# Kernel optimization log

Measured on AMD Instinct MI355X. Metric: run time of the kernel, lower is better.

Reference implementation:

```python
import jax, jax.numpy as jnp
import numpy as np

D_MODEL, D_K, D_V = 1024, 64, 64
B, S = 4, 4096


def setup_inputs() -> dict:
    key = jax.random.key(0)
    ks = jax.random.split(key, 13)
    s = 1.0 / np.sqrt(D_MODEL)
    inp = {
        "q": jax.random.normal(ks[0], (B, S, D_MODEL), jnp.float32),
        "k": jax.random.normal(ks[1], (B, S, D_MODEL), jnp.float32),
        "v": jax.random.normal(ks[2], (B, S, D_MODEL), jnp.float32),
        "mask": jax.random.randint(ks[3], (1, S, S), 0, 2, jnp.int32),
        "Wq": jax.random.normal(ks[4], (D_K, D_MODEL), jnp.float32) * s,
        "bq": jax.random.normal(ks[5], (D_K,), jnp.float32) * s,
        "Wk": jax.random.normal(ks[6], (D_K, D_MODEL), jnp.float32) * s,
        "bk": jax.random.normal(ks[7], (D_K,), jnp.float32) * s,
        "Wv": jax.random.normal(ks[8], (D_V, D_MODEL), jnp.float32) * s,
        "bv": jax.random.normal(ks[9], (D_V,), jnp.float32) * s,
        "Wo": jax.random.normal(ks[10], (D_MODEL, D_V), jnp.float32) / np.sqrt(D_V),
        "bo": jax.random.normal(ks[11], (D_MODEL,), jnp.float32) / np.sqrt(D_V),
    }
    return inp


def reference(q, k, v, mask, Wq, bq, Wk, bk, Wv, bv, Wo, bo):
    # linear projections (torch Linear: x @ W.T + b)
    qh = jnp.einsum("bsd,kd->bsk", q, Wq) + bq   # [B,S,d_k]
    kh = jnp.einsum("bsd,kd->bsk", k, Wk) + bk   # [B,S,d_k]
    vh = jnp.einsum("bsd,vd->bsv", v, Wv) + bv   # [B,S,d_v]
    scale = 1.0 / jnp.sqrt(jnp.float32(D_K))
    scores = jnp.einsum("bqk,bmk->bqm", qh, kh) * scale  # [B,S,S]
    scores = jnp.where(mask == 0, jnp.float32(-1e9), scores)
    attn = jax.nn.softmax(scores, axis=-1)
    out = jnp.einsum("bqm,bmv->bqv", attn, vh)   # [B,S,d_v]
    return jnp.einsum("bqv,dv->bqd", out, Wo) + bo
```

## Files before the change

### kernel.cpp

```cpp
#include <hip/hip_runtime.h>
#include <cmath>

typedef __attribute__((ext_vector_type(8))) short bf16x8;
typedef __attribute__((ext_vector_type(4))) short bf16x4;
typedef __attribute__((ext_vector_type(4))) float f32x4;

constexpr int B_ = 4;
constexpr int S_ = 4096;
constexpr int DM_ = 1024;
constexpr int DK_ = 64;
constexpr int NROW = B_ * S_;

__device__ __forceinline__ short f2bf(float x) {
  union { float f; unsigned u; } c; c.f = x;
  unsigned r = (c.u + 0x7FFF + ((c.u >> 16) & 1)) >> 16;
  return (short)r;
}
__device__ __forceinline__ float bf2f(short h) {
  union { float f; unsigned u; } c; c.u = ((unsigned)(unsigned short)h) << 16;
  return c.f;
}

__global__ __launch_bounds__(256) void prep(
    const int* __restrict__ mask, unsigned long long* __restrict__ bits,
    const float* __restrict__ Wq, const float* __restrict__ Wk,
    const float* __restrict__ Wv, short* __restrict__ wbf) {
  if (blockIdx.x < 1024) {
    const int wid = (blockIdx.x * 256 + threadIdx.x) >> 6;
    const int lane = threadIdx.x & 63;
    const size_t base = (size_t)wid * 4096;
    for (int it = 0; it < 64; ++it) {
      int m = mask[base + it * 64 + lane];
      unsigned long long b = __ballot(m != 0);
      if (lane == 0) bits[(size_t)wid * 64 + it] = b;
    }
  } else {
    const int mat = blockIdx.x - 1024;
    const float* W = mat == 0 ? Wq : (mat == 1 ? Wk : Wv);
    short* dst = wbf + (size_t)mat * DK_ * DM_;
    const int t = threadIdx.x;
#pragma unroll 4
    for (int i = 0; i < 32; ++i) {
      int idx = i * 2048 + t * 8;
      f32x4 a0 = *(const f32x4*)(W + idx);
      f32x4 a1 = *(const f32x4*)(W + idx + 4);
      bf16x8 h;
#pragma unroll
      for (int j = 0; j < 4; ++j) { h[j] = f2bf(a0[j]); h[j + 4] = f2bf(a1[j]); }
      *(bf16x8*)(dst + idx) = h;
    }
  }
}

__global__ __launch_bounds__(256, 3) void proj_mfma(
    const float* __restrict__ q, const float* __restrict__ k,
    const float* __restrict__ v, const short* __restrict__ wbf,
    const float* __restrict__ bq, const float* __restrict__ bk,
    const float* __restrict__ bv,
    short* __restrict__ qh, short* __restrict__ kh, short* __restrict__ vhT) {
  const int mat = blockIdx.z;
  const float* X    = mat == 0 ? q : (mat == 1 ? k : v);
  const short* W    = wbf + (size_t)mat * DK_ * DM_;
  const float* bias = mat == 0 ? bq : (mat == 1 ? bk : bv);

  const int t = threadIdx.x;
  const int row0 = blockIdx.x * 64;
  const int lane = t & 63, w = t >> 6, quad = lane >> 4, l16 = lane & 15;

  const int myrow = row0 + 16 * w + l16;
  const float* xp = X + (size_t)myrow * DM_ + quad * 8;
  const short* wp0 = W + (size_t)l16 * DM_ + quad * 8;
  const short* wp1 = wp0 + 16 * DM_;
  const short* wp2 = wp0 + 32 * DM_;
  const short* wp3 = wp0 + 48 * DM_;

  f32x4 acc[4] = {};
  f32x4 xr[4][4];

#pragma unroll
  for (int pb = 0; pb < 3; ++pb) {
    const float* s = xp + pb * 64;
    xr[pb][0] = *(const f32x4*)(s + 0);
    xr[pb][1] = *(const f32x4*)(s + 4);
    xr[pb][2] = *(const f32x4*)(s + 32);
    xr[pb][3] = *(const f32x4*)(s + 36);
  }

#pragma unroll 4
  for (int ks = 0; ks < 16; ++ks) {
    if (ks < 13) {
      const float* s = xp + (ks + 3) * 64;
      xr[(ks + 3) & 3][0] = *(const f32x4*)(s + 0);
      xr[(ks + 3) & 3][1] = *(const f32x4*)(s + 4);
      xr[(ks + 3) & 3][2] = *(const f32x4*)(s + 32);
      xr[(ks + 3) & 3][3] = *(const f32x4*)(s + 36);
    }

    bf16x8 wf[2][4];
#pragma unroll
    for (int c = 0; c < 2; ++c) {
      wf[c][0] = *(const bf16x8*)(wp0 + ks * 64 + c * 32);
      wf[c][1] = *(const bf16x8*)(wp1 + ks * 64 + c * 32);
      wf[c][2] = *(const bf16x8*)(wp2 + ks * 64 + c * 32);
      wf[c][3] = *(const bf16x8*)(wp3 + ks * 64 + c * 32);
    }

#pragma unroll
    for (int c = 0; c < 2; ++c) {
      f32x4 x0 = xr[ks & 3][2 * c + 0];
      f32x4 x1 = xr[ks & 3][2 * c + 1];
      bf16x8 ahi, alo;
#pragma unroll
      for (int j = 0; j < 4; ++j) {
        short h0 = f2bf(x0[j]); ahi[j] = h0;     alo[j]     = f2bf(x0[j] - bf2f(h0));
        short h1 = f2bf(x1[j]); ahi[j + 4] = h1; alo[j + 4] = f2bf(x1[j] - bf2f(h1));
      }
#pragma unroll
      for (int ct = 0; ct < 4; ++ct) {
        acc[ct] = __builtin_amdgcn_mfma_f32_16x16x32_bf16(ahi, wf[c][ct], acc[ct], 0, 0, 0);
        acc[ct] = __builtin_amdgcn_mfma_f32_16x16x32_bf16(alo, wf[c][ct], acc[ct], 0, 0, 0);
      }
    }
  }

  float bs[4];
#pragma unroll
  for (int ct = 0; ct < 4; ++ct) bs[ct] = bias[16 * ct + l16];

  short* dstq = (mat == 0) ? qh : kh;
#pragma unroll
  for (int ct = 0; ct < 4; ++ct)
#pragma unroll
    for (int reg = 0; reg < 4; ++reg) {
      int r = row0 + 16 * w + quad * 4 + reg;
      int c = 16 * ct + l16;
      short hv = f2bf(acc[ct][reg] + bs[ct]);
      if (mat == 2)
        vhT[((size_t)(r >> 12) * DK_ + c) * S_ + (r & 4095)] = hv;
      else
        dstq[(size_t)r * DK_ + c] = hv;
    }
}

__global__ __launch_bounds__(256) void attn_mfma(
    const short* __restrict__ qh, const short* __restrict__ kh,
    const short* __restrict__ vhT, const unsigned int* __restrict__ mbits,
    float* __restrict__ Opart, float* __restrict__ mpart,
    float* __restrict__ lpart, int ns) {
  __shared__ short ks[64][72];
  __shared__ short vt[64][72];
  __shared__ short ps[4][16][72];

  const int b = blockIdx.z;
  const int split = blockIdx.y;
  const int q0 = blockIdx.x * 64;
  const int t = threadIdx.x, lane = t & 63, w = t >> 6;
  const int quad = lane >> 4, l16 = lane & 15;
  const int myq = q0 + 16 * w + l16;

  const int kt0 = split * (S_ / ns);
  const int kt1 = kt0 + S_ / ns;

  bf16x8 qf[2];
  {
    const short* src = qh + ((size_t)b * S_ + myq) * DK_ + quad * 8;
    qf[0] = *(const bf16x8*)src;
    qf[1] = *(const bf16x8*)(src + 32);
  }

  f32x4 ao[4] = {};
  float m_i = -INFINITY, l_i = 0.0f;

  const int sr = t >> 2;
  const int sseg = t & 3;

  for (int kt = kt0; kt < kt1; kt += 64) {
    __syncthreads();
    {
      const short* srck = kh + ((size_t)b * S_ + kt + sr) * DK_;
      *(bf16x8*)&ks[sr][8 * sseg]       = *(const bf16x8*)(srck + 8 * sseg);
      *(bf16x8*)&ks[sr][8 * (sseg + 4)] = *(const bf16x8*)(srck + 8 * (sseg + 4));
      const short* srcv = vhT + ((size_t)b * DK_ + sr) * S_ + kt;
      *(bf16x8*)&vt[sr][8 * sseg]       = *(const bf16x8*)(srcv + 8 * sseg);
      *(bf16x8*)&vt[sr][8 * (sseg + 4)] = *(const bf16x8*)(srcv + 8 * (sseg + 4));
    }
    const uint2 mw = *(const uint2*)&mbits[(size_t)myq * 128 + (kt >> 5)];
    __syncthreads();

    f32x4 sacc[4] = {};
#pragma unroll
    for (int c = 0; c < 2; ++c)
#pragma unroll
      for (int tt = 0; tt < 4; ++tt) {
        bf16x8 a = *(const bf16x8*)&ks[16 * tt + l16][c * 32 + quad * 8];
        sacc[tt] = __builtin_amdgcn_mfma_f32_16x16x32_bf16(a, qf[c], sacc[tt], 0, 0, 0);
      }

    float sc[16];
#pragma unroll
    for (int tt = 0; tt < 4; ++tt) {
      unsigned wrd = (tt & 2) ? mw.y : mw.x;
      int base = (tt & 1) * 16 + quad * 4;
#pragma unroll
      for (int r = 0; r < 4; ++r)
        sc[tt * 4 + r] = ((wrd >> (base + r)) & 1) ? sacc[tt][r] * 0.125f : -1e9f;
    }

    float mx = sc[0];
#pragma unroll
    for (int i = 1; i < 16; ++i) mx = fmaxf(mx, sc[i]);
    mx = fmaxf(mx, __shfl_xor(mx, 16));
    mx = fmaxf(mx, __shfl_xor(mx, 32));
    float m_new = fmaxf(m_i, mx);
    float alpha = __expf(m_i - m_new);
    float p[16], sum = 0.0f;
#pragma unroll
    for (int i = 0; i < 16; ++i) { p[i] = __expf(sc[i] - m_new); sum += p[i]; }
    sum += __shfl_xor(sum, 16);
    sum += __shfl_xor(sum, 32);
    l_i = l_i * alpha + sum;
    m_i = m_new;

#pragma unroll
    for (int tt = 0; tt < 4; ++tt) {
      bf16x4 pk;
#pragma unroll
      for (int r = 0; r < 4; ++r) pk[r] = f2bf(p[tt * 4 + r]);
      *(bf16x4*)&ps[w][l16][16 * tt + quad * 4] = pk;
    }

#pragma unroll
    for (int dt = 0; dt < 4; ++dt)
#pragma unroll
      for (int r = 0; r < 4; ++r) ao[dt][r] *= alpha;

#pragma unroll
    for (int c = 0; c < 2; ++c) {
      bf16x8 bp = *(const bf16x8*)&ps[w][l16][c * 32 + quad * 8];
#pragma unroll
      for (int dt = 0; dt < 4; ++dt) {
        bf16x8 av = *(const bf16x8*)&vt[16 * dt + l16][c * 32 + quad * 8];
        ao[dt] = __builtin_amdgcn_mfma_f32_16x16x32_bf16(av, bp, ao[dt], 0, 0, 0);
      }
    }
  }

  const size_t prow = (size_t)split * NROW + (size_t)b * S_ + myq;
#pragma unroll
  for (int dt = 0; dt < 4; ++dt)
    *(f32x4*)&Opart[prow * DK_ + 16 * dt + quad * 4] = ao[dt];
  if (quad == 0) {
    mpart[prow] = m_i;
    lpart[prow] = l_i;
  }
}

__global__ __launch_bounds__(256) void attn_combine(
    const float* __restrict__ Opart, const float* __restrict__ mpart,
    const float* __restrict__ lpart, short* __restrict__ o_bf, int ns) {
  const int t = threadIdx.x;
  const int row = blockIdx.x * 64 + (t >> 2);
  const int c0 = (t & 3) * 16;

  float M = -INFINITY;
  for (int s = 0; s < ns; ++s) M = fmaxf(M, mpart[(size_t)s * NROW + row]);
  float L = 0.0f, wt[4];
  for (int s = 0; s < ns; ++s) {
    wt[s] = __expf(mpart[(size_t)s * NROW + row] - M);
    L += wt[s] * lpart[(size_t)s * NROW + row];
  }
  float acc[16] = {};
  for (int s = 0; s < ns; ++s) {
    const float* src = Opart + ((size_t)s * NROW + row) * DK_ + c0;
#pragma unroll
    for (int j = 0; j < 16; j += 4) {
      f32x4 vv = *(const f32x4*)(src + j);
#pragma unroll
      for (int r = 0; r < 4; ++r) acc[j + r] += wt[s] * vv[r];
    }
  }
  const float inv = 1.0f / L;
  bf16x8 o0, o1;
#pragma unroll
  for (int j = 0; j < 8; ++j) {
    o0[j] = f2bf(acc[j] * inv);
    o1[j] = f2bf(acc[j + 8] * inv);
  }
  *(bf16x8*)&o_bf[(size_t)row * DK_ + c0]     = o0;
  *(bf16x8*)&o_bf[(size_t)row * DK_ + c0 + 8] = o1;
}

__global__ __launch_bounds__(256) void outproj_mfma(
    const short* __restrict__ o_bf, const float* __restrict__ Wo,
    const float* __restrict__ bo, float* __restrict__ out) {
  __shared__ short os[64][72];
  __shared__ short wos[256][72];

  const int t = threadIdx.x, lane = t & 63, w = t >> 6;
  const int quad = lane >> 4, l16 = lane & 15;
  const int s0 = blockIdx.y * 64;
  const int dm0 = blockIdx.x * 256;

  {
    int r = t >> 2, cq = (t & 3) * 16;
    const short* src = o_bf + (size_t)(s0 + r) * DK_ + cq;
    *(bf16x8*)&os[r][cq]     = *(const bf16x8*)src;
    *(bf16x8*)&os[r][cq + 8] = *(const bf16x8*)(src + 8);
  }
#pragma unroll
  for (int pass = 0; pass < 4; ++pass) {
    int r = pass * 64 + (t >> 2), cq = (t & 3) * 16;
    const float* src = Wo + (size_t)(dm0 + r) * DK_ + cq;
    f32x4 a0 = *(const f32x4*)src, a1 = *(const f32x4*)(src + 4);
    f32x4 a2 = *(const f32x4*)(src + 8), a3 = *(const f32x4*)(src + 12);
    bf16x8 v0, v1;
#pragma unroll
    for (int j = 0; j < 4; ++j) {
      v0[j] = f2bf(a0[j]); v0[j + 4] = f2bf(a1[j]);
      v1[j] = f2bf(a2[j]); v1[j + 4] = f2bf(a3[j]);
    }
    *(bf16x8*)&wos[r][cq]     = v0;
    *(bf16x8*)&wos[r][cq + 8] = v1;
  }
  __syncthreads();

  bf16x8 af[2];
#pragma unroll
  for (int c = 0; c < 2; ++c)
    af[c] = *(const bf16x8*)&os[16 * w + l16][c * 32 + quad * 8];

  f32x4 acc[16] = {};
#pragma unroll
  for (int c = 0; c < 2; ++c)
#pragma unroll
    for (int nt = 0; nt < 16; ++nt) {
      bf16x8 bw = *(const bf16x8*)&wos[16 * nt + l16][c * 32 + quad * 8];
      acc[nt] = __builtin_amdgcn_mfma_f32_16x16x32_bf16(af[c], bw, acc[nt], 0, 0, 0);
    }

  float bias_r[16];
#pragma unroll
  for (int nt = 0; nt < 16; ++nt) bias_r[nt] = bo[dm0 + 16 * nt + l16];

#pragma unroll
  for (int nt = 0; nt < 16; ++nt)
#pragma unroll
    for (int reg = 0; reg < 4; ++reg) {
      int s = s0 + 16 * w + quad * 4 + reg;
      int dm = dm0 + 16 * nt + l16;
      out[(size_t)s * DM_ + dm] = acc[nt][reg] + bias_r[nt];
    }
}

extern "C" void kernel_launch(void* const* d_in, const int* in_sizes, int n_in,
                              void* d_out, int out_size, void* d_ws,
                              size_t ws_size, hipStream_t stream) {
  (void)in_sizes; (void)n_in; (void)out_size;
  const float* q  = (const float*)d_in[0];
  const float* k  = (const float*)d_in[1];
  const float* v  = (const float*)d_in[2];
  const int* mask = (const int*)d_in[3];
  const float* Wq = (const float*)d_in[4];
  const float* bq = (const float*)d_in[5];
  const float* Wk = (const float*)d_in[6];
  const float* bk = (const float*)d_in[7];
  const float* Wv = (const float*)d_in[8];
  const float* bv = (const float*)d_in[9];
  const float* Wo = (const float*)d_in[10];
  const float* bo = (const float*)d_in[11];
  float* out = (float*)d_out;

  short* qh  = (short*)d_ws;
  short* kh  = qh + (size_t)NROW * DK_;
  short* vhT = kh + (size_t)NROW * DK_;
  unsigned int* mbits = (unsigned int*)(vhT + (size_t)NROW * DK_);
  short* o_bf = (short*)(mbits + (size_t)S_ * 128);
  float* mpart = (float*)(o_bf + (size_t)NROW * DK_);
  float* lpart = mpart + 4 * NROW;
  float* Opart = lpart + 4 * NROW;
  short* wbf = (short*)Opart;

  const size_t base_bytes = (size_t)((char*)Opart - (char*)d_ws);
  const size_t per_split = (size_t)NROW * DK_ * sizeof(float);
  int ns = 1;
  if (ws_size >= base_bytes + 4 * per_split) ns = 4;
  else if (ws_size >= base_bytes + 2 * per_split) ns = 2;

  prep<<<1027, 256, 0, stream>>>(mask, (unsigned long long*)mbits,
                                 Wq, Wk, Wv, wbf);
  proj_mfma<<<dim3(NROW / 64, 1, 3), 256, 0, stream>>>(
      q, k, v, wbf, bq, bk, bv, qh, kh, vhT);
  attn_mfma<<<dim3(S_ / 64, ns, B_), 256, 0, stream>>>(
      qh, kh, vhT, mbits, Opart, mpart, lpart, ns);
  attn_combine<<<NROW / 64, 256, 0, stream>>>(Opart, mpart, lpart, o_bf, ns);
  outproj_mfma<<<dim3(DM_ / 256, NROW / 64), 256, 0, stream>>>(o_bf, Wo, bo, out);
}
```

Before: 390.1 us.

## Stage projection weights through swizzled double-buffered LDS via async global_load_lds

The projection kernel used to load bf16 weight fragments directly from global memory in every wave, each k-step. It now cooperatively copies each 64x64 weight slice into a double-buffered, XOR-swizzled LDS tile with global_load_lds, overlapped with the X prefetch and the MFMA work, and uses explicit vmcnt waits and barriers between stages. This is meant to cut redundant global/L2 weight traffic across the four waves and hide its latency. The cost is block-level barriers each step and hand-tuned waitcnt counts that could be fragile. The X prefetch depth also drops from 3 to 2 slices.

New measurement: 373.0 us. 1.05x faster.

```diff
diff --git a/kernel.cpp b/kernel.cpp
--- a/kernel.cpp
+++ b/kernel.cpp
@@ -4,6 +4,9 @@
 typedef __attribute__((ext_vector_type(8))) short bf16x8;
 typedef __attribute__((ext_vector_type(4))) short bf16x4;
 typedef __attribute__((ext_vector_type(4))) float f32x4;
+typedef unsigned int u32;
+typedef __attribute__((address_space(1))) const u32 gu32;
+typedef __attribute__((address_space(3))) u32 lu32;
 
 constexpr int B_ = 4;
 constexpr int S_ = 4096;
@@ -19,6 +22,9 @@
 __device__ __forceinline__ float bf2f(short h) {
   union { float f; unsigned u; } c; c.u = ((unsigned)(unsigned short)h) << 16;
   return c.f;
+}
+__device__ __forceinline__ void gl16(const void* g, void* l) {
+  __builtin_amdgcn_global_load_lds((gu32*)g, (lu32*)l, 16, 0, 0);
 }
 
 __global__ __launch_bounds__(256) void prep(
@@ -58,6 +64,8 @@
     const float* __restrict__ bq, const float* __restrict__ bk,
     const float* __restrict__ bv,
     short* __restrict__ qh, short* __restrict__ kh, short* __restrict__ vhT) {
+  __shared__ short wlds[2][64][64];
+
   const int mat = blockIdx.z;
   const float* X    = mat == 0 ? q : (mat == 1 ? k : v);
   const short* W    = wbf + (size_t)mat * DK_ * DM_;
@@ -69,46 +77,48 @@
 
   const int myrow = row0 + 16 * w + l16;
   const float* xp = X + (size_t)myrow * DM_ + quad * 8;
-  const short* wp0 = W + (size_t)l16 * DM_ + quad * 8;
-  const short* wp1 = wp0 + 16 * DM_;
-  const short* wp2 = wp0 + 32 * DM_;
-  const short* wp3 = wp0 + 48 * DM_;
+
+  const int grA = 16 * w + (lane >> 3);
+  const int scolh = (((lane & 7) ^ (lane >> 3)) * 8);
+  const short* wsrcA = W + (size_t)grA * DM_ + scolh;
+  const short* wsrcB = W + (size_t)(grA + 8) * DM_ + scolh;
+  short* wdstA0 = &wlds[0][16 * w][0] + lane * 8;
+  short* wdstB0 = &wlds[0][16 * w + 8][0] + lane * 8;
+  short* wdstA1 = &wlds[1][16 * w][0] + lane * 8;
+  short* wdstB1 = &wlds[1][16 * w + 8][0] + lane * 8;
+
+  const int rsw = (l16 & 7) << 4;
 
   f32x4 acc[4] = {};
   f32x4 xr[4][4];
 
-#pragma unroll
-  for (int pb = 0; pb < 3; ++pb) {
+  gl16(wsrcA, wdstA0);
+  gl16(wsrcB, wdstB0);
+#pragma unroll
+  for (int pb = 0; pb < 2; ++pb) {
     const float* s = xp + pb * 64;
     xr[pb][0] = *(const f32x4*)(s + 0);
     xr[pb][1] = *(const f32x4*)(s + 4);
     xr[pb][2] = *(const f32x4*)(s + 32);
     xr[pb][3] = *(const f32x4*)(s + 36);
   }
-
-#pragma unroll 4
-  for (int ks = 0; ks < 16; ++ks) {
-    if (ks < 13) {
-      const float* s = xp + (ks + 3) * 64;
-      xr[(ks + 3) & 3][0] = *(const f32x4*)(s + 0);
-      xr[(ks + 3) & 3][1] = *(const f32x4*)(s + 4);
-      xr[(ks + 3) & 3][2] = *(const f32x4*)(s + 32);
-      xr[(ks + 3) & 3][3] = *(const f32x4*)(s + 36);
-    }
-
+  asm volatile("s_waitcnt vmcnt(8)" ::: "memory");
+  __builtin_amdgcn_s_barrier();
+  __builtin_amdgcn_sched_barrier(0);
+
+  auto compute_step = [&](int i, int buf) {
+    const char* wb = (const char*)&wlds[buf][0][0];
     bf16x8 wf[2][4];
 #pragma unroll
+    for (int c = 0; c < 2; ++c)
+#pragma unroll
+      for (int ct = 0; ct < 4; ++ct)
+        wf[c][ct] = *(const bf16x8*)(wb + (16 * ct + l16) * 128 +
+                                     ((c * 64 + quad * 16) ^ rsw));
+#pragma unroll
     for (int c = 0; c < 2; ++c) {
-      wf[c][0] = *(const bf16x8*)(wp0 + ks * 64 + c * 32);
-      wf[c][1] = *(const bf16x8*)(wp1 + ks * 64 + c * 32);
-      wf[c][2] = *(const bf16x8*)(wp2 + ks * 64 + c * 32);
-      wf[c][3] = *(const bf16x8*)(wp3 + ks * 64 + c * 32);
-    }
-
-#pragma unroll
-    for (int c = 0; c < 2; ++c) {
-      f32x4 x0 = xr[ks & 3][2 * c + 0];
-      f32x4 x1 = xr[ks & 3][2 * c + 1];
+      f32x4 x0 = xr[i & 3][2 * c + 0];
+      f32x4 x1 = xr[i & 3][2 * c + 1];
       bf16x8 ahi, alo;
 #pragma unroll
       for (int j = 0; j < 4; ++j) {
@@ -121,7 +131,55 @@
         acc[ct] = __builtin_amdgcn_mfma_f32_16x16x32_bf16(alo, wf[c][ct], acc[ct], 0, 0, 0);
       }
     }
-  }
+  };
+
+#pragma unroll 4
+  for (int i = 0; i < 12; ++i) {
+    const int nb = (i + 1) & 1;
+    gl16(wsrcA + (i + 1) * 64, nb ? wdstA1 : wdstA0);
+    gl16(wsrcB + (i + 1) * 64, nb ? wdstB1 : wdstB0);
+    {
+      const float* s = xp + (i + 2) * 64;
+      xr[(i + 2) & 3][0] = *(const f32x4*)(s + 0);
+      xr[(i + 2) & 3][1] = *(const f32x4*)(s + 4);
+      xr[(i + 2) & 3][2] = *(const f32x4*)(s + 32);
+      xr[(i + 2) & 3][3] = *(const f32x4*)(s + 36);
+    }
+    compute_step(i, i & 1);
+    asm volatile("s_waitcnt vmcnt(4)" ::: "memory");
+    __builtin_amdgcn_s_barrier();
+    __builtin_amdgcn_sched_barrier(0);
+  }
+
+  gl16(wsrcA + 13 * 64, wdstA1);
+  gl16(wsrcB + 13 * 64, wdstB1);
+  {
+    const float* s = xp + 14 * 64;
+    xr[2][0] = *(const f32x4*)(s + 0);  xr[2][1] = *(const f32x4*)(s + 4);
+    xr[2][2] = *(const f32x4*)(s + 32); xr[2][3] = *(const f32x4*)(s + 36);
+  }
+  compute_step(12, 0);
+  asm volatile("s_waitcnt vmcnt(4)" ::: "memory");
+  __builtin_amdgcn_s_barrier();
+  __builtin_amdgcn_sched_barrier(0);
+  gl16(wsrcA + 14 * 64, wdstA0);
+  gl16(wsrcB + 14 * 64, wdstB0);
+  {
+    const float* s = xp + 15 * 64;
+    xr[3][0] = *(const f32x4*)(s + 0);  xr[3][1] = *(const f32x4*)(s + 4);
+    xr[3][2] = *(const f32x4*)(s + 32); xr[3][3] = *(const f32x4*)(s + 36);
+  }
+  compute_step(13, 1);
+  asm volatile("s_waitcnt vmcnt(4)" ::: "memory");
+  __builtin_amdgcn_s_barrier();
+  __builtin_amdgcn_sched_barrier(0);
+  gl16(wsrcA + 15 * 64, wdstA1);
+  gl16(wsrcB + 15 * 64, wdstB1);
+  compute_step(14, 0);
+  asm volatile("s_waitcnt vmcnt(0)" ::: "memory");
+  __builtin_amdgcn_s_barrier();
+  __builtin_amdgcn_sched_barrier(0);
+  compute_step(15, 1);
 
   float bs[4];
 #pragma unroll
```
